# Kernel optimization log

Measured on AMD Instinct MI355X. Metric: run time of the kernel, lower is better.

## Reference

```python
import jax, jax.numpy as jnp
import numpy as np


def setup_inputs() -> dict:
    key = jax.random.key(0)
    kq, kk, kv, km = jax.random.split(key, 4)
    B, H, S, D = 2, 16, 2048, 64
    Q = jax.random.normal(kq, (B, H, S, D), dtype=jnp.float32)
    K = jax.random.normal(kk, (B, H, S, D), dtype=jnp.float32)
    V = jax.random.normal(kv, (B, H, S, D), dtype=jnp.float32)
    mask = jax.random.randint(km, (B, 1, S, S), 0, 2).astype(jnp.bool_)
    return {"Q": Q, "K": K, "V": V, "mask": mask}


def reference(Q, K, V, mask):
    # scores: [B, H, Sq, Sk]
    scores = jnp.einsum("bhqd,bhkd->bhqk", Q, K)
    neg = jnp.finfo(scores.dtype).min
    # Faithful to original: mask fill happens BEFORE the sqrt(d) scaling.
    scores = jnp.where(mask, neg, scores)
    inv_sqrt_d = 1.0 / jnp.sqrt(jnp.asarray(Q.shape[-1], dtype=scores.dtype))
    attn = jax.nn.softmax(scores * inv_sqrt_d, axis=-1)
    return jnp.einsum("bhqk,bhkd->bhqd", attn, V)
```

## Files before the change

kernel.cpp:

```cpp
#include <hip/hip_runtime.h>
#include <stdint.h>


#define SQ 2048
#define DH 64

using bf16x8  = __attribute__((ext_vector_type(8)))  __bf16;
using f32x4   = __attribute__((ext_vector_type(4)))  float;
using ushort8 = __attribute__((ext_vector_type(8)))  unsigned short;
using ushort4v= __attribute__((ext_vector_type(4)))  unsigned short;

static __device__ __forceinline__ unsigned short f2bf(float f) {
    union { float f; uint32_t u; } c; c.f = f;
    return (unsigned short)((c.u + 0x8000u) >> 16);
}

static __device__ __forceinline__ int swz(int row, int col) {
    return row * 64 + ((((col >> 3) ^ (row & 7))) << 3) + (col & 7);
}

static __device__ __forceinline__ f32x4 mfma16(bf16x8 a, bf16x8 b, f32x4 c) {
    return __builtin_amdgcn_mfma_f32_16x16x32_bf16(a, b, c, 0, 0, 0);
}

static __device__ __forceinline__ void gload16(const void* g, void* l) {
    __builtin_amdgcn_global_load_lds(
        (const __attribute__((address_space(1))) void*)g,
        (__attribute__((address_space(3))) void*)l, 16, 0, 0);
}

__global__ void pack_mask_kernel(const int* __restrict__ mask,
                                 unsigned long long* __restrict__ words, int nwords) {
    int gid = blockIdx.x * blockDim.x + threadIdx.x;
    int w = gid >> 6;
    int l = gid & 63;
    if (w < nwords) {
        int mv = mask[(size_t)w * 64 + l];
        unsigned long long b = __ballot(mv != 0);
        if (l == 0) words[w] = b;
    }
}

__global__ void cvt_bf16_kernel(const float* __restrict__ src,
                                unsigned short* __restrict__ dst) {
    int gid = blockIdx.x * blockDim.x + threadIdx.x;
    float4 v = ((const float4*)src)[gid];
    ushort4v t;
    t[0] = f2bf(v.x); t[1] = f2bf(v.y); t[2] = f2bf(v.z); t[3] = f2bf(v.w);
    ((ushort4v*)dst)[gid] = t;
}

__global__ __launch_bounds__(256)
void vtrans_kernel(const float* __restrict__ V, unsigned short* __restrict__ Vt) {
    __shared__ unsigned short tl[64][66];
    const int tid = threadIdx.x;
    const int kt  = blockIdx.x & 31;
    const size_t bh = blockIdx.x >> 5;
    const float* vp = V + (bh * SQ + (size_t)kt * 64) * DH;
    #pragma unroll
    for (int i = 0; i < 4; ++i) {
        int idx = tid + 256 * i;
        int key = idx >> 4;
        int dc  = (idx & 15) * 4;
        float4 v = *(const float4*)(vp + (size_t)key * DH + dc);
        tl[key][dc + 0] = f2bf(v.x);
        tl[key][dc + 1] = f2bf(v.y);
        tl[key][dc + 2] = f2bf(v.z);
        tl[key][dc + 3] = f2bf(v.w);
    }
    __syncthreads();
    unsigned short* op = Vt + bh * DH * SQ + (size_t)kt * 64;
    #pragma unroll
    for (int i = 0; i < 4; ++i) {
        int idx = tid + 256 * i;
        int d  = idx >> 4;
        int kc = (idx & 15) * 4;
        ushort4v t;
        t[0] = tl[kc + 0][d]; t[1] = tl[kc + 1][d];
        t[2] = tl[kc + 2][d]; t[3] = tl[kc + 3][d];
        *(ushort4v*)(op + (size_t)d * SQ + kc) = t;
    }
}

__global__ __launch_bounds__(256, 4)
void attn_kernel(const float* __restrict__ Q,
                 const unsigned short* __restrict__ Kb,
                 const unsigned short* __restrict__ Vtg,
                 const unsigned long long* __restrict__ Mw,
                 float* __restrict__ out) {
    __shared__ __align__(16) unsigned short Ks[2][64 * 64];
    __shared__ __align__(16) unsigned short Vs[2][64 * 64];
    __shared__ __align__(16) unsigned short Ps[4 * 16 * 64];

    const int tid  = threadIdx.x;
    const int w    = tid >> 6;
    const int l    = tid & 63;
    const int quad = l >> 4;
    const int c16  = l & 15;
    const int bx = blockIdx.x;
    const int hh = bx & 15;
    const int b  = (bx >> 4) & 1;
    const int qt = bx >> 5;

    const size_t bh = (size_t)b * 16 + hh;
    const float* Qp = Q + bh * SQ * DH;
    const int qw = qt * 64 + 16 * w;
    const unsigned long long* Mq = Mw + ((size_t)b * SQ + qw + quad * 4) * (SQ / 64);

    const int s0 = (2 * w) * 64 + l;
    const int s1 = (2 * w + 1) * 64 + l;
    const int r0 = s0 >> 3, g0 = s0 & 7;
    const int r1 = s1 >> 3, g1 = s1 & 7;
    const char* Kg = (const char*)(Kb  + bh * (size_t)SQ * DH);
    const char* Vg = (const char*)(Vtg + bh * (size_t)DH * SQ);
    const char* kSrc0 = Kg + r0 * 128  + ((g0 ^ (r0 & 7)) << 4);
    const char* kSrc1 = Kg + r1 * 128  + ((g1 ^ (r1 & 7)) << 4);
    const char* vSrc0 = Vg + r0 * 4096 + ((g0 ^ (r0 & 7)) << 4);
    const char* vSrc1 = Vg + r1 * 4096 + ((g1 ^ (r1 & 7)) << 4);

    bf16x8 qf[2];
    {
        const float* qr = Qp + (size_t)(qw + c16) * DH;
        #pragma unroll
        for (int c = 0; c < 2; ++c) {
            int d0 = 32 * c + 8 * quad;
            float4 a  = *(const float4*)(qr + d0);
            float4 b4 = *(const float4*)(qr + d0 + 4);
            ushort8 t;
            t[0]=f2bf(a.x);  t[1]=f2bf(a.y);  t[2]=f2bf(a.z);  t[3]=f2bf(a.w);
            t[4]=f2bf(b4.x); t[5]=f2bf(b4.y); t[6]=f2bf(b4.z); t[7]=f2bf(b4.w);
            qf[c] = __builtin_bit_cast(bf16x8, t);
        }
    }

    f32x4 o[4];
    float lsum[4];
    #pragma unroll
    for (int i = 0; i < 4; ++i) { o[i] = (f32x4)(0.f); lsum[i] = 0.f; }

    unsigned short* Pw = Ps + w * (16 * 64);
    const int xg = (c16 & 7);

    unsigned long long mws[4];
    #pragma unroll
    for (int r = 0; r < 4; ++r) mws[r] = Mq[(size_t)r * (SQ / 64)];

    gload16(kSrc0, &Ks[0][(2 * w) * 512]);
    gload16(kSrc1, &Ks[0][(2 * w + 1) * 512]);
    gload16(vSrc0, &Vs[0][(2 * w) * 512]);
    gload16(vSrc1, &Vs[0][(2 * w + 1) * 512]);
    kSrc0 += 8192; kSrc1 += 8192; vSrc0 += 128; vSrc1 += 128;
    __syncthreads();

    for (int t = 0; t < 32; ++t) {
        const int cur = t & 1;

        unsigned long long nmws[4];
        if (t < 31) {
            gload16(kSrc0, &Ks[cur ^ 1][(2 * w) * 512]);
            gload16(kSrc1, &Ks[cur ^ 1][(2 * w + 1) * 512]);
            gload16(vSrc0, &Vs[cur ^ 1][(2 * w) * 512]);
            gload16(vSrc1, &Vs[cur ^ 1][(2 * w + 1) * 512]);
            kSrc0 += 8192; kSrc1 += 8192; vSrc0 += 128; vSrc1 += 128;
            #pragma unroll
            for (int r = 0; r < 4; ++r) nmws[r] = Mq[(size_t)r * (SQ / 64) + (t + 1)];
        }

        const unsigned short* Kc = Ks[cur];
        const unsigned short* Vc = Vs[cur];

        f32x4 s[4];
        #pragma unroll
        for (int i = 0; i < 4; ++i) s[i] = (f32x4)(0.f);
        #pragma unroll
        for (int c = 0; c < 2; ++c) {
            int g = ((4 * c + quad) ^ xg) << 3;
            #pragma unroll
            for (int nb = 0; nb < 4; ++nb) {
                bf16x8 kb = __builtin_bit_cast(bf16x8,
                    *(const ushort8*)&Kc[(c16 + 16 * nb) * 64 + g]);
                s[nb] = mfma16(qf[c], kb, s[nb]);
            }
        }

        #pragma unroll
        for (int r = 0; r < 4; ++r) {
            int row = quad * 4 + r;
            unsigned lo = (unsigned)mws[r];
            unsigned hi = (unsigned)(mws[r] >> 32);
            #pragma unroll
            for (int nb = 0; nb < 4; ++nb) {
                float e = __builtin_amdgcn_exp2f(fmaf(s[nb][r], 0.18033688f, -5.7707802f));
                unsigned bits = (nb & 2) ? hi : lo;
                unsigned bit  = 1u << (c16 + 16 * (nb & 1));
                float pv = (bits & bit) ? 0.0f : e;
                lsum[r] += pv;
                Pw[swz(row, c16 + 16 * nb)] = f2bf(pv);
            }
        }

        bf16x8 pa[2];
        #pragma unroll
        for (int c = 0; c < 2; ++c)
            pa[c] = __builtin_bit_cast(bf16x8,
                *(const ushort8*)&Pw[c16 * 64 + (((4 * c + quad) ^ xg) << 3)]);
        #pragma unroll
        for (int c = 0; c < 2; ++c) {
            int g = ((4 * c + quad) ^ xg) << 3;
            #pragma unroll
            for (int db = 0; db < 4; ++db) {
                bf16x8 vb = __builtin_bit_cast(bf16x8,
                    *(const ushort8*)&Vc[(c16 + 16 * db) * 64 + g]);
                o[db] = mfma16(pa[c], vb, o[db]);
            }
        }

        __syncthreads();
        if (t < 31) {
            #pragma unroll
            for (int r = 0; r < 4; ++r) mws[r] = nmws[r];
        }
    }

    #pragma unroll
    for (int r = 0; r < 4; ++r) {
        float v = lsum[r];
        v += __shfl_xor(v, 1, 64);
        v += __shfl_xor(v, 2, 64);
        v += __shfl_xor(v, 4, 64);
        v += __shfl_xor(v, 8, 64);
        float rinv = 1.0f / v;
        float* op = out + (bh * SQ + (size_t)(qw + quad * 4 + r)) * DH + c16;
        #pragma unroll
        for (int db = 0; db < 4; ++db) op[16 * db] = o[db][r] * rinv;
    }
}

extern "C" void kernel_launch(void* const* d_in, const int* in_sizes, int n_in,
                              void* d_out, int out_size, void* d_ws, size_t ws_size,
                              hipStream_t stream) {
    const float* Q    = (const float*)d_in[0];
    const float* K    = (const float*)d_in[1];
    const float* V    = (const float*)d_in[2];
    const int*   mask = (const int*)d_in[3];
    float* out = (float*)d_out;

    char* ws = (char*)d_ws;
    unsigned long long* mwords = (unsigned long long*)ws;
    unsigned short* Kb = (unsigned short*)(ws + (1 << 20));
    unsigned short* Vt = (unsigned short*)(ws + (1 << 20) + (8 << 20));

    const int nwords = 2 * SQ * (SQ / 64);
    pack_mask_kernel<<<dim3((nwords * 64) / 256), dim3(256), 0, stream>>>(mask, mwords, nwords);
    cvt_bf16_kernel<<<dim3(4096), dim3(256), 0, stream>>>(K, Kb);
    vtrans_kernel<<<dim3(1024), dim3(256), 0, stream>>>(V, Vt);
    attn_kernel<<<dim3(1024), dim3(256), 0, stream>>>(Q, Kb, Vt, mwords, out);
}
```

Before: 189.2 us.

## Fuse prep kernels into one launch and interleave softmax with PV MFMAs

Merges the mask-packing, K bf16 conversion and V transpose kernels into a single block-indexed prep kernel, cutting two kernel launches and their serialization gaps. In the attention loop, the P computation is split into two halves so the first PV MFMA chunk can issue while the second half's exponentials are computed. It also adds s_setprio around MFMA groups, precomputes LDS offsets, and uses a native bf16 conversion for P. The risk is that the unified prep kernel carries the larger V-transpose LDS footprint for every block, and the bf16 conversion rounding mode differs slightly.

New measurement: 189.2 us. No clear change (-0.0%).

```diff
diff --git a/kernel.cpp b/kernel.cpp
--- a/kernel.cpp
+++ b/kernel.cpp
@@ -15,6 +15,10 @@
     return (unsigned short)((c.u + 0x8000u) >> 16);
 }
 
+static __device__ __forceinline__ unsigned short bfr(float f) {
+    return __builtin_bit_cast(unsigned short, (__bf16)f);
+}
+
 static __device__ __forceinline__ int swz(int row, int col) {
     return row * 64 + ((((col >> 3) ^ (row & 7))) << 3) + (col & 7);
 }
@@ -29,56 +33,52 @@
         (__attribute__((address_space(3))) void*)l, 16, 0, 0);
 }
 
-__global__ void pack_mask_kernel(const int* __restrict__ mask,
-                                 unsigned long long* __restrict__ words, int nwords) {
-    int gid = blockIdx.x * blockDim.x + threadIdx.x;
-    int w = gid >> 6;
-    int l = gid & 63;
-    if (w < nwords) {
-        int mv = mask[(size_t)w * 64 + l];
+__global__ __launch_bounds__(256)
+void prep_kernel(const int* __restrict__ mask, const float* __restrict__ K,
+                 const float* __restrict__ V, unsigned long long* __restrict__ words,
+                 unsigned short* __restrict__ Kb, unsigned short* __restrict__ Vt) {
+    __shared__ unsigned short tl[64][66];
+    const int bx  = blockIdx.x;
+    const int tid = threadIdx.x;
+    if (bx < 32768) {
+        int gid = bx * 256 + tid;
+        int mv = mask[gid];
         unsigned long long b = __ballot(mv != 0);
-        if (l == 0) words[w] = b;
-    }
-}
-
-__global__ void cvt_bf16_kernel(const float* __restrict__ src,
-                                unsigned short* __restrict__ dst) {
-    int gid = blockIdx.x * blockDim.x + threadIdx.x;
-    float4 v = ((const float4*)src)[gid];
-    ushort4v t;
-    t[0] = f2bf(v.x); t[1] = f2bf(v.y); t[2] = f2bf(v.z); t[3] = f2bf(v.w);
-    ((ushort4v*)dst)[gid] = t;
-}
-
-__global__ __launch_bounds__(256)
-void vtrans_kernel(const float* __restrict__ V, unsigned short* __restrict__ Vt) {
-    __shared__ unsigned short tl[64][66];
-    const int tid = threadIdx.x;
-    const int kt  = blockIdx.x & 31;
-    const size_t bh = blockIdx.x >> 5;
-    const float* vp = V + (bh * SQ + (size_t)kt * 64) * DH;
-    #pragma unroll
-    for (int i = 0; i < 4; ++i) {
-        int idx = tid + 256 * i;
-        int key = idx >> 4;
-        int dc  = (idx & 15) * 4;
-        float4 v = *(const float4*)(vp + (size_t)key * DH + dc);
-        tl[key][dc + 0] = f2bf(v.x);
-        tl[key][dc + 1] = f2bf(v.y);
-        tl[key][dc + 2] = f2bf(v.z);
-        tl[key][dc + 3] = f2bf(v.w);
-    }
-    __syncthreads();
-    unsigned short* op = Vt + bh * DH * SQ + (size_t)kt * 64;
-    #pragma unroll
-    for (int i = 0; i < 4; ++i) {
-        int idx = tid + 256 * i;
-        int d  = idx >> 4;
-        int kc = (idx & 15) * 4;
+        if ((gid & 63) == 0) words[gid >> 6] = b;
+    } else if (bx < 36864) {
+        int gid = (bx - 32768) * 256 + tid;
+        float4 v = ((const float4*)K)[gid];
         ushort4v t;
-        t[0] = tl[kc + 0][d]; t[1] = tl[kc + 1][d];
-        t[2] = tl[kc + 2][d]; t[3] = tl[kc + 3][d];
-        *(ushort4v*)(op + (size_t)d * SQ + kc) = t;
+        t[0]=f2bf(v.x); t[1]=f2bf(v.y); t[2]=f2bf(v.z); t[3]=f2bf(v.w);
+        ((ushort4v*)Kb)[gid] = t;
+    } else {
+        const int vbx = bx - 36864;
+        const int kt  = vbx & 31;
+        const size_t bh = vbx >> 5;
+        const float* vp = V + (bh * SQ + (size_t)kt * 64) * DH;
+        #pragma unroll
+        for (int i = 0; i < 4; ++i) {
+            int idx = tid + 256 * i;
+            int key = idx >> 4;
+            int dc  = (idx & 15) * 4;
+            float4 v = *(const float4*)(vp + (size_t)key * DH + dc);
+            tl[key][dc + 0] = f2bf(v.x);
+            tl[key][dc + 1] = f2bf(v.y);
+            tl[key][dc + 2] = f2bf(v.z);
+            tl[key][dc + 3] = f2bf(v.w);
+        }
+        __syncthreads();
+        unsigned short* op = Vt + bh * DH * SQ + (size_t)kt * 64;
+        #pragma unroll
+        for (int i = 0; i < 4; ++i) {
+            int idx = tid + 256 * i;
+            int d  = idx >> 4;
+            int kc = (idx & 15) * 4;
+            ushort4v t;
+            t[0] = tl[kc + 0][d]; t[1] = tl[kc + 1][d];
+            t[2] = tl[kc + 2][d]; t[3] = tl[kc + 3][d];
+            *(ushort4v*)(op + (size_t)d * SQ + kc) = t;
+        }
     }
 }
 
@@ -109,14 +109,14 @@
 
     const int s0 = (2 * w) * 64 + l;
     const int s1 = (2 * w + 1) * 64 + l;
-    const int r0 = s0 >> 3, g0 = s0 & 7;
-    const int r1 = s1 >> 3, g1 = s1 & 7;
+    const int r0 = s0 >> 3, g0s = s0 & 7;
+    const int r1 = s1 >> 3, g1s = s1 & 7;
     const char* Kg = (const char*)(Kb  + bh * (size_t)SQ * DH);
     const char* Vg = (const char*)(Vtg + bh * (size_t)DH * SQ);
-    const char* kSrc0 = Kg + r0 * 128  + ((g0 ^ (r0 & 7)) << 4);
-    const char* kSrc1 = Kg + r1 * 128  + ((g1 ^ (r1 & 7)) << 4);
-    const char* vSrc0 = Vg + r0 * 4096 + ((g0 ^ (r0 & 7)) << 4);
-    const char* vSrc1 = Vg + r1 * 4096 + ((g1 ^ (r1 & 7)) << 4);
+    const char* kSrc0 = Kg + r0 * 128  + ((g0s ^ (r0 & 7)) << 4);
+    const char* kSrc1 = Kg + r1 * 128  + ((g1s ^ (r1 & 7)) << 4);
+    const char* vSrc0 = Vg + r0 * 4096 + ((g0s ^ (r0 & 7)) << 4);
+    const char* vSrc1 = Vg + r1 * 4096 + ((g1s ^ (r1 & 7)) << 4);
 
     bf16x8 qf[2];
     {
@@ -141,6 +141,20 @@
     unsigned short* Pw = Ps + w * (16 * 64);
     const int xg = (c16 & 7);
 
+    const unsigned bit0 = 1u << c16;
+    const unsigned bit1 = 1u << (c16 + 16);
+    int poff[4][4];
+    #pragma unroll
+    for (int r = 0; r < 4; ++r)
+        #pragma unroll
+        for (int nb = 0; nb < 4; ++nb)
+            poff[r][nb] = swz(quad * 4 + r, c16 + 16 * nb);
+    int gfrag[2];
+    #pragma unroll
+    for (int c = 0; c < 2; ++c) gfrag[c] = ((4 * c + quad) ^ xg) << 3;
+    const int paoff0 = c16 * 64 + gfrag[0];
+    const int paoff1 = c16 * 64 + gfrag[1];
+
     unsigned long long mws[4];
     #pragma unroll
     for (int r = 0; r < 4; ++r) mws[r] = Mq[(size_t)r * (SQ / 64)];
@@ -172,47 +186,63 @@
         f32x4 s[4];
         #pragma unroll
         for (int i = 0; i < 4; ++i) s[i] = (f32x4)(0.f);
+        __builtin_amdgcn_s_setprio(1);
         #pragma unroll
         for (int c = 0; c < 2; ++c) {
-            int g = ((4 * c + quad) ^ xg) << 3;
             #pragma unroll
             for (int nb = 0; nb < 4; ++nb) {
                 bf16x8 kb = __builtin_bit_cast(bf16x8,
-                    *(const ushort8*)&Kc[(c16 + 16 * nb) * 64 + g]);
+                    *(const ushort8*)&Kc[(c16 + 16 * nb) * 64 + gfrag[c]]);
                 s[nb] = mfma16(qf[c], kb, s[nb]);
             }
         }
+        __builtin_amdgcn_s_setprio(0);
+
 
         #pragma unroll
         for (int r = 0; r < 4; ++r) {
-            int row = quad * 4 + r;
             unsigned lo = (unsigned)mws[r];
-            unsigned hi = (unsigned)(mws[r] >> 32);
-            #pragma unroll
-            for (int nb = 0; nb < 4; ++nb) {
-                float e = __builtin_amdgcn_exp2f(fmaf(s[nb][r], 0.18033688f, -5.7707802f));
-                unsigned bits = (nb & 2) ? hi : lo;
-                unsigned bit  = 1u << (c16 + 16 * (nb & 1));
-                float pv = (bits & bit) ? 0.0f : e;
-                lsum[r] += pv;
-                Pw[swz(row, c16 + 16 * nb)] = f2bf(pv);
-            }
-        }
-
-        bf16x8 pa[2];
-        #pragma unroll
-        for (int c = 0; c < 2; ++c)
-            pa[c] = __builtin_bit_cast(bf16x8,
-                *(const ushort8*)&Pw[c16 * 64 + (((4 * c + quad) ^ xg) << 3)]);
-        #pragma unroll
-        for (int c = 0; c < 2; ++c) {
-            int g = ((4 * c + quad) ^ xg) << 3;
+            float p0 = (lo & bit0) ? 0.0f
+                     : __builtin_amdgcn_exp2f(fmaf(s[0][r], 0.18033688f, -5.7707802f));
+            float p1 = (lo & bit1) ? 0.0f
+                     : __builtin_amdgcn_exp2f(fmaf(s[1][r], 0.18033688f, -5.7707802f));
+            lsum[r] += p0 + p1;
+            Pw[poff[r][0]] = bfr(p0);
+            Pw[poff[r][1]] = bfr(p1);
+        }
+        {
+            bf16x8 pa0 = __builtin_bit_cast(bf16x8, *(const ushort8*)&Pw[paoff0]);
+            __builtin_amdgcn_s_setprio(1);
             #pragma unroll
             for (int db = 0; db < 4; ++db) {
                 bf16x8 vb = __builtin_bit_cast(bf16x8,
-                    *(const ushort8*)&Vc[(c16 + 16 * db) * 64 + g]);
-                o[db] = mfma16(pa[c], vb, o[db]);
+                    *(const ushort8*)&Vc[(c16 + 16 * db) * 64 + gfrag[0]]);
+                o[db] = mfma16(pa0, vb, o[db]);
             }
+            __builtin_amdgcn_s_setprio(0);
+        }
+
+        #pragma unroll
+        for (int r = 0; r < 4; ++r) {
+            unsigned hi = (unsigned)(mws[r] >> 32);
+            float p2 = (hi & bit0) ? 0.0f
+                     : __builtin_amdgcn_exp2f(fmaf(s[2][r], 0.18033688f, -5.7707802f));
+            float p3 = (hi & bit1) ? 0.0f
+                     : __builtin_amdgcn_exp2f(fmaf(s[3][r], 0.18033688f, -5.7707802f));
+            lsum[r] += p2 + p3;
+            Pw[poff[r][2]] = bfr(p2);
+            Pw[poff[r][3]] = bfr(p3);
+        }
+        {
+            bf16x8 pa1 = __builtin_bit_cast(bf16x8, *(const ushort8*)&Pw[paoff1]);
+            __builtin_amdgcn_s_setprio(1);
+            #pragma unroll
+            for (int db = 0; db < 4; ++db) {
+                bf16x8 vb = __builtin_bit_cast(bf16x8,
+                    *(const ushort8*)&Vc[(c16 + 16 * db) * 64 + gfrag[1]]);
+                o[db] = mfma16(pa1, vb, o[db]);
+            }
+            __builtin_amdgcn_s_setprio(0);
         }
 
         __syncthreads();
@@ -250,9 +280,6 @@
     unsigned short* Kb = (unsigned short*)(ws + (1 << 20));
     unsigned short* Vt = (unsigned short*)(ws + (1 << 20) + (8 << 20));
 
-    const int nwords = 2 * SQ * (SQ / 64);
-    pack_mask_kernel<<<dim3((nwords * 64) / 256), dim3(256), 0, stream>>>(mask, mwords, nwords);
-    cvt_bf16_kernel<<<dim3(4096), dim3(256), 0, stream>>>(K, Kb);
-    vtrans_kernel<<<dim3(1024), dim3(256), 0, stream>>>(V, Vt);
+    prep_kernel<<<dim3(37888), dim3(256), 0, stream>>>(mask, K, V, mwords, Kb, Vt);
     attn_kernel<<<dim3(1024), dim3(256), 0, stream>>>(Q, Kb, Vt, mwords, out);
 }
```
